# Optimization experiments

Measured on AMD Instinct MI355X. Metric: run time of the kernel, lower is better.

## Reference

```python
import jax, jax.numpy as jnp
import numpy as np
import math

B, S, D, H, NB = 32, 512, 512, 8, 2
DK = D // H
DF = 4 * D
EPS = 1e-8


def layer_norm(x, gamma, beta):
    # Matches torch: unbiased std (ddof=1), divide by (std + eps)
    mean = jnp.mean(x, axis=-1, keepdims=True)
    std = jnp.sqrt(jnp.var(x, axis=-1, keepdims=True, ddof=1))
    return gamma * (x - mean) / (std + EPS) + beta


def block(x, wq, bq, wk, bk, wv, bv, wr, br, ga, ba, wc1, bc1, wc2, bc2, gf, bf):
    # --- attention with ReLU-gated Q/K/V ---
    Q = jax.nn.relu(x @ wq.T + bq)  # [B,S,D]
    K = jax.nn.relu(x @ wk.T + bk)
    V = jax.nn.relu(x @ wv.T + bv)
    # chunk along last dim -> heads; head-major stacking is equivalent to this reshape
    Qh = Q.reshape(B, S, H, DK)
    Kh = K.reshape(B, S, H, DK)
    Vh = V.reshape(B, S, H, DK)
    scores = jnp.einsum('bqhd,bkhd->bhqk', Qh, Kh) / math.sqrt(DK)
    w = jax.nn.softmax(scores, axis=-1)
    out = jnp.einsum('bhqk,bkhd->bqhd', w, Vh).reshape(B, S, D)
    out = out + jax.nn.relu(x @ wr.T + br)
    out = layer_norm(out, ga, ba)
    # --- conv1d (kernel=1) feed-forward ---
    h = jax.nn.relu(out @ wc1.T + bc1)  # [B,S,4D]
    y = h @ wc2.T + bc2                 # [B,S,D]
    y = layer_norm(y + out, gf, bf)
    return y


def setup_inputs() -> dict:
    key = jax.random.key(0)
    ks = jax.random.split(key, 8)
    std = 0.01
    inp = {
        'x': jax.random.normal(ks[0], (B, S, D), jnp.float32),
        'wq': jax.random.normal(ks[1], (NB, D, D), jnp.float32) * std,
        'bq': jnp.zeros((NB, D), jnp.float32),
        'wk': jax.random.normal(ks[2], (NB, D, D), jnp.float32) * std,
        'bk': jnp.zeros((NB, D), jnp.float32),
        'wv': jax.random.normal(ks[3], (NB, D, D), jnp.float32) * std,
        'bv': jnp.zeros((NB, D), jnp.float32),
        'wr': jax.random.normal(ks[4], (NB, D, D), jnp.float32) * std,
        'br': jnp.zeros((NB, D), jnp.float32),
        'g_attn': jnp.ones((NB, D), jnp.float32),
        'b_attn': jnp.zeros((NB, D), jnp.float32),
        'wc1': jax.random.normal(ks[5], (NB, DF, D), jnp.float32) * (1.0 / math.sqrt(D)),
        'bc1': jnp.zeros((NB, DF), jnp.float32),
        'wc2': jax.random.normal(ks[6], (NB, D, DF), jnp.float32) * (1.0 / math.sqrt(DF)),
        'bc2': jnp.zeros((NB, D), jnp.float32),
        'g_ffn': jnp.ones((NB, D), jnp.float32),
        'b_ffn': jnp.zeros((NB, D), jnp.float32),
    }
    return inp


def reference(x, wq, bq, wk, bk, wv, bv, wr, br, g_attn, b_attn,
              wc1, bc1, wc2, bc2, g_ffn, b_ffn):
    enc = x
    for i in range(NB):
        enc = block(enc, wq[i], bq[i], wk[i], bk[i], wv[i], bv[i], wr[i], br[i],
                    g_attn[i], b_attn[i], wc1[i], bc1[i], wc2[i], bc2[i],
                    g_ffn[i], b_ffn[i])
    return enc
```

## Files before the change

kernel.cpp:

```cpp
#include <hip/hip_runtime.h>

typedef unsigned short u16;
typedef __bf16 bf16x8 __attribute__((ext_vector_type(8)));
typedef float f32x4 __attribute__((ext_vector_type(4)));
typedef unsigned short ushort8 __attribute__((ext_vector_type(8)));

__device__ __forceinline__ void gload_lds16(const void* g, void* l) {
  __builtin_amdgcn_global_load_lds(
      (const __attribute__((address_space(1))) void*)g,
      (__attribute__((address_space(3))) void*)l, 16, 0, 0);
}

__device__ __forceinline__ u16 f2bf(float f) {
  unsigned int u = __builtin_bit_cast(unsigned int, f);
  u = (u + 0x7fffu + ((u >> 16) & 1u)) >> 16;
  return (u16)u;
}
__device__ __forceinline__ u16 f2bf_trunc(float f) {
  return (u16)(__builtin_bit_cast(unsigned int, f) >> 16);
}
__device__ __forceinline__ float bf2f(u16 u) {
  unsigned int v = (unsigned int)u << 16;
  return __builtin_bit_cast(float, v);
}

__global__ void castk(const float* __restrict__ in, u16* __restrict__ out, int n,
                      float scale) {
  size_t i = ((size_t)blockIdx.x * 256 + threadIdx.x) * 8;
  if (i >= (size_t)n) return;
  const float4* p = (const float4*)(in + i);
  float4 a = p[0], b = p[1];
  ushort8 o;
  o[0] = f2bf(a.x * scale); o[1] = f2bf(a.y * scale);
  o[2] = f2bf(a.z * scale); o[3] = f2bf(a.w * scale);
  o[4] = f2bf(b.x * scale); o[5] = f2bf(b.y * scale);
  o[6] = f2bf(b.z * scale); o[7] = f2bf(b.w * scale);
  *(ushort8*)(out + i) = o;
}

__global__ void castw4(const float* __restrict__ w0, const float* __restrict__ w1,
                       const float* __restrict__ w2, const float* __restrict__ w3,
                       u16* __restrict__ out) {
  size_t idx = ((size_t)blockIdx.x * 256 + threadIdx.x) * 8;
  int i = (int)(idx >> 20);
  int j = (int)((idx >> 18) & 3);
  int e = (int)(idx & 262143);
  const float* src = (j == 0) ? w0 : (j == 1) ? w1 : (j == 2) ? w2 : w3;
  float scale = (j == 0) ? 0.125f : 1.0f;
  const float4* p = (const float4*)(src + (size_t)i * 262144 + e);
  float4 a = p[0], b = p[1];
  ushort8 o;
  o[0] = f2bf(a.x * scale); o[1] = f2bf(a.y * scale);
  o[2] = f2bf(a.z * scale); o[3] = f2bf(a.w * scale);
  o[4] = f2bf(b.x * scale); o[5] = f2bf(b.y * scale);
  o[6] = f2bf(b.z * scale); o[7] = f2bf(b.w * scale);
  *(ushort8*)(out + idx) = o;
}

__global__ void biasg(const float* __restrict__ b0, const float* __restrict__ b1,
                      const float* __restrict__ b2, const float* __restrict__ b3,
                      float* __restrict__ out) {
  int idx = blockIdx.x * 256 + threadIdx.x;
  int i = idx >> 11, j = (idx >> 9) & 3, c = idx & 511;
  const float* src = (j == 0) ? b0 : (j == 1) ? b1 : (j == 2) ? b2 : b3;
  float v = src[i * 512 + c];
  out[idx] = (j == 0) ? v * 0.125f : v;
}

template<int RELU, int WVT>
__global__ __launch_bounds__(256, 4)
void gemm97(const u16* __restrict__ A, const u16* __restrict__ W,
            const float* __restrict__ bias, u16* __restrict__ C,
            u16* __restrict__ VT, int M, int N, int K)
{
  __shared__ char lds[32768];
  char* ABase = lds;
  char* BBase = lds + 16384;

  const int tid = threadIdx.x, w = tid >> 6, l = tid & 63;
  const int l15 = l & 15, lh = l >> 4;
  const int nbn = N >> 7;
  const int p = blockIdx.x;
  const int bm = (p & 7) * 16 + (p >> 3) / nbn;
  const int bn = (p >> 3) % nbn;
  const int wm = w >> 1, wn = w & 1;
  const int NT = K >> 6;

  const int srow = l >> 3;
  const int scol = ((l & 7) ^ srow) << 3;
  const u16* aG = A + (size_t)(bm * 128 + srow) * K + scol;
  const u16* bG = W + (size_t)(bn * 128 + srow) * K + scol;

  auto stage = [&](int t) {
#pragma unroll
    for (int i = 0; i < 4; ++i) {
      int c = w * 4 + i;
      gload_lds16(aG + (size_t)(c * 8) * K + t * 64, ABase + c * 1024);
      gload_lds16(bG + (size_t)(c * 8) * K + t * 64, BBase + c * 1024);
    }
  };

  f32x4 acc[4][4] = {};

  for (int t = 0; t < NT; ++t) {
    __syncthreads();
    stage(t);
    __syncthreads();
    bf16x8 a[4], b[4];
#pragma unroll
    for (int kk = 0; kk < 2; ++kk) {
#pragma unroll
      for (int mf = 0; mf < 4; ++mf) {
        int row = wm * 64 + mf * 16 + l15;
        a[mf] = *(const bf16x8*)(ABase + row * 128 +
                 ((kk * 64 + lh * 16) ^ ((row & 7) << 4)));
      }
#pragma unroll
      for (int nf = 0; nf < 4; ++nf) {
        int row = wn * 64 + nf * 16 + l15;
        b[nf] = *(const bf16x8*)(BBase + row * 128 +
                 ((kk * 64 + lh * 16) ^ ((row & 7) << 4)));
      }
      __builtin_amdgcn_s_setprio(1);
#pragma unroll
      for (int mf = 0; mf < 4; ++mf)
#pragma unroll
        for (int nf = 0; nf < 4; ++nf)
          acc[mf][nf] = __builtin_amdgcn_mfma_f32_16x16x32_bf16(a[mf], b[nf], acc[mf][nf], 0, 0, 0);
      __builtin_amdgcn_s_setprio(0);
    }
  }

  __syncthreads();
  char* Ct = (char*)lds;
  const int rowL = wm * 64 + (lh << 2);
  const int colL = wn * 64 + l15;
  const bool dovt = WVT && (bn >= 8) && (bn < 12);
  float bv[4];
#pragma unroll
  for (int nf = 0; nf < 4; ++nf) bv[nf] = bias[bn * 128 + colL + nf * 16];

  if (!dovt) {
#pragma unroll
    for (int mf = 0; mf < 4; ++mf)
#pragma unroll
      for (int nf = 0; nf < 4; ++nf)
#pragma unroll
        for (int r = 0; r < 4; ++r) {
          float v = acc[mf][nf][r] + bv[nf];
          if (RELU) v = fmaxf(v, 0.f);
          int m = rowL + mf * 16 + r, n = colL + nf * 16;
          *(u16*)(Ct + m * 256 + ((n * 2) ^ ((m & 7) << 4))) = f2bf(v);
        }
    __syncthreads();
#pragma unroll
    for (int pass = 0; pass < 8; ++pass) {
      int row = pass * 16 + (tid >> 4);
      int c16 = tid & 15;
      bf16x8 vv = *(const bf16x8*)(Ct + row * 256 + ((c16 * 16) ^ ((row & 7) << 4)));
      *(bf16x8*)(&C[(size_t)(bm * 128 + row) * N + bn * 128 + c16 * 8]) = vv;
    }
  } else {
#pragma unroll
    for (int mf = 0; mf < 4; ++mf)
#pragma unroll
      for (int nf = 0; nf < 4; ++nf)
#pragma unroll
        for (int r = 0; r < 4; ++r) {
          float v = acc[mf][nf][r] + bv[nf];
          if (RELU) v = fmaxf(v, 0.f);
          int m = rowL + mf * 16 + r, d = colL + nf * 16;
          *(u16*)(Ct + d * 256 + ((m * 2) ^ ((d & 7) << 4))) = f2bf(v);
        }
    __syncthreads();
    const int batch = bm >> 2;
#pragma unroll
    for (int pass = 0; pass < 8; ++pass) {
      int dL = pass * 16 + (tid >> 4);
      int m16 = tid & 15;
      bf16x8 vv = *(const bf16x8*)(Ct + dL * 256 + ((m16 * 16) ^ ((dL & 7) << 4)));
      int head = (bn - 8) * 2 + (dL >> 6);
      int vtr = (batch * 8 + head) * 64 + (dL & 63);
      *(bf16x8*)(&VT[(size_t)vtr * 512 + (bm & 3) * 128 + m16 * 8]) = vv;
    }
  }
}

__global__ __launch_bounds__(256, 3)
void attn_kernel(const u16* __restrict__ qkvr, const u16* __restrict__ VT,
                 u16* __restrict__ F)
{
  const int D4 = 2048;
  __shared__ u16 QPs[128 * 64];
  __shared__ u16 Ks[2][64 * 64];
  __shared__ u16 Vs[2][64 * 64];

  const int tid = threadIdx.x, w = tid >> 6, l = tid & 63;
  const int bh = blockIdx.x & 255, qt = blockIdx.x >> 8;
  const int b = bh >> 3, h = bh & 7;
  const int lr = l >> 3, lc = ((l & 7) ^ lr) << 3;
  const int l15 = l & 15, lh = l >> 4;

  const u16* qG = qkvr + (size_t)(b * 512 + qt * 128) * D4 + h * 64 + lc;
#pragma unroll
  for (int i = 0; i < 4; ++i) {
    int c = w * 4 + i;
    gload_lds16(qG + (size_t)(c * 8 + lr) * D4, &QPs[c * 512]);
  }

  const u16* kG = qkvr + (size_t)(b * 512) * D4 + 512 + h * 64 + lc;
  const u16* vG = VT + (size_t)(bh * 64) * 512 + lc;

  auto stageKV = [&](int kt) {
    const int bsel = kt & 1;
#pragma unroll
    for (int i = 0; i < 2; ++i) {
      int c = w * 2 + i;
      gload_lds16(kG + (size_t)(kt * 64 + c * 8 + lr) * D4, &Ks[bsel][c * 512]);
      gload_lds16(vG + (size_t)(c * 8 + lr) * 512 + kt * 64, &Vs[bsel][c * 512]);
    }
  };
  stageKV(0);
  __syncthreads();

  bf16x8 qa[2][2];
#pragma unroll
  for (int kk = 0; kk < 2; ++kk)
#pragma unroll
    for (int qq = 0; qq < 2; ++qq) {
      int qrow = w * 32 + qq * 16 + l15;
      qa[kk][qq] = *(const bf16x8*)((const char*)QPs + qrow * 128 +
                    ((kk * 64 + (lh << 4)) ^ ((qrow & 7) << 4)));
    }

  f32x4 o_acc[2][4] = {};
  float psum[2][4] = {};

  for (int kt = 0; kt < 8; ++kt) {
    if (kt) __syncthreads();
    if (kt < 7) stageKV(kt + 1);
    const char* Kb = (const char*)Ks[kt & 1];
    const char* Vb = (const char*)Vs[kt & 1];

    f32x4 sacc[2][4] = {};
#pragma unroll
    for (int kk = 0; kk < 2; ++kk) {
#pragma unroll
      for (int ni = 0; ni < 4; ++ni) {
        int krow = ni * 16 + l15;
        bf16x8 kb = *(const bf16x8*)(Kb + krow * 128 +
                    ((kk * 64 + (lh << 4)) ^ ((krow & 7) << 4)));
#pragma unroll
        for (int qq = 0; qq < 2; ++qq)
          sacc[qq][ni] = __builtin_amdgcn_mfma_f32_16x16x32_bf16(qa[kk][qq], kb, sacc[qq][ni], 0, 0, 0);
      }
    }

#pragma unroll
    for (int qq = 0; qq < 2; ++qq)
#pragma unroll
      for (int r = 0; r < 4; ++r) {
        float p0 = __expf(sacc[qq][0][r]);
        float p1 = __expf(sacc[qq][1][r]);
        float p2 = __expf(sacc[qq][2][r]);
        float p3 = __expf(sacc[qq][3][r]);
        psum[qq][r] += (p0 + p1) + (p2 + p3);
        int q = w * 32 + qq * 16 + (lh << 2) + r;
        int sw = (q & 7) << 4;
        int col = l15 * 2;
        char* pb = (char*)QPs + q * 128;
        *(u16*)(pb + ((0  + col) ^ sw)) = f2bf_trunc(p0);
        *(u16*)(pb + ((32 + col) ^ sw)) = f2bf_trunc(p1);
        *(u16*)(pb + ((64 + col) ^ sw)) = f2bf_trunc(p2);
        *(u16*)(pb + ((96 + col) ^ sw)) = f2bf_trunc(p3);
      }

#pragma unroll
    for (int kk = 0; kk < 2; ++kk) {
      bf16x8 pa[2];
#pragma unroll
      for (int qq = 0; qq < 2; ++qq) {
        int qrow = w * 32 + qq * 16 + l15;
        pa[qq] = *(const bf16x8*)((const char*)QPs + qrow * 128 +
                  ((kk * 64 + (lh << 4)) ^ ((qrow & 7) << 4)));
      }
#pragma unroll
      for (int ni = 0; ni < 4; ++ni) {
        int d = ni * 16 + l15;
        bf16x8 vb = *(const bf16x8*)(Vb + d * 128 +
                    ((kk * 64 + (lh << 4)) ^ ((d & 7) << 4)));
#pragma unroll
        for (int qq = 0; qq < 2; ++qq)
          o_acc[qq][ni] = __builtin_amdgcn_mfma_f32_16x16x32_bf16(pa[qq], vb, o_acc[qq][ni], 0, 0, 0);
      }
    }
  }

  float lsum[2][4];
#pragma unroll
  for (int qq = 0; qq < 2; ++qq)
#pragma unroll
    for (int r = 0; r < 4; ++r) {
      float t = psum[qq][r];
#pragma unroll
      for (int m = 1; m < 16; m <<= 1) t += __shfl_xor(t, m);
      lsum[qq][r] = 1.f / t;
    }

#pragma unroll
  for (int qq = 0; qq < 2; ++qq)
#pragma unroll
    for (int ni = 0; ni < 4; ++ni) {
      int d = ni * 16 + l15;
#pragma unroll
      for (int r = 0; r < 4; ++r) {
        float v = o_acc[qq][ni][r] * lsum[qq][r];
        int q = w * 32 + qq * 16 + (lh << 2) + r;
        *(u16*)((char*)QPs + q * 128 + ((d * 2) ^ ((q & 7) << 4))) = f2bf(v);
      }
    }
  __syncthreads();
  const u16* Rbase = qkvr + (size_t)(b * 512 + qt * 128) * D4 + 1536 + h * 64;
  u16* Fbase = F + (size_t)(b * 512 + qt * 128) * 512 + h * 64;
#pragma unroll
  for (int pass = 0; pass < 4; ++pass) {
    int row = pass * 32 + (tid >> 3), c8 = tid & 7;
    ushort8 lv = *(const ushort8*)((char*)QPs + row * 128 + ((c8 * 16) ^ ((row & 7) << 4)));
    ushort8 rv = *(const ushort8*)(Rbase + (size_t)row * D4 + c8 * 8);
    ushort8 o;
#pragma unroll
    for (int j = 0; j < 8; ++j) o[j] = f2bf(bf2f(lv[j]) + bf2f(rv[j]));
    *(ushort8*)(Fbase + (size_t)row * 512 + c8 * 8) = o;
  }
}

template<int HAS_RES, int OUT_F32>
__global__ __launch_bounds__(256)
void ln_bf(const u16* __restrict__ in, const u16* __restrict__ res,
           const float* __restrict__ gamma, const float* __restrict__ beta,
           u16* __restrict__ outb, float* __restrict__ outf)
{
  const int l = threadIdx.x & 63;
  const size_t row = (size_t)blockIdx.x * 4 + (threadIdx.x >> 6);
  ushort8 iv = *(const ushort8*)(in + row * 512 + l * 8);
  float x[8];
#pragma unroll
  for (int j = 0; j < 8; ++j) x[j] = bf2f(iv[j]);
  if (HAS_RES) {
    ushort8 rv = *(const ushort8*)(res + row * 512 + l * 8);
#pragma unroll
    for (int j = 0; j < 8; ++j) x[j] += bf2f(rv[j]);
  }
  float s = 0.f, ss = 0.f;
#pragma unroll
  for (int j = 0; j < 8; ++j) { s += x[j]; ss += x[j] * x[j]; }
#pragma unroll
  for (int m = 1; m < 64; m <<= 1) { s += __shfl_xor(s, m); ss += __shfl_xor(ss, m); }
  float mean = s * (1.f / 512.f);
  float var = fmaxf((ss - 512.f * mean * mean) * (1.f / 511.f), 0.f);
  float inv = 1.f / (sqrtf(var) + 1e-8f);
  const float4* g4 = (const float4*)gamma;
  const float4* b4 = (const float4*)beta;
  float4 g0 = g4[l * 2], g1 = g4[l * 2 + 1];
  float4 b0 = b4[l * 2], b1 = b4[l * 2 + 1];
  float gg[8] = {g0.x, g0.y, g0.z, g0.w, g1.x, g1.y, g1.z, g1.w};
  float bb[8] = {b0.x, b0.y, b0.z, b0.w, b1.x, b1.y, b1.z, b1.w};
  float y[8];
#pragma unroll
  for (int j = 0; j < 8; ++j) y[j] = gg[j] * (x[j] - mean) * inv + bb[j];
  if (outb) {
    ushort8 o;
#pragma unroll
    for (int j = 0; j < 8; ++j) o[j] = f2bf(y[j]);
    *(ushort8*)(outb + row * 512 + l * 8) = o;
  }
  if (OUT_F32) {
    float4* o4 = (float4*)(outf + row * 512);
    o4[l * 2]     = make_float4(y[0], y[1], y[2], y[3]);
    o4[l * 2 + 1] = make_float4(y[4], y[5], y[6], y[7]);
  }
}

extern "C" void kernel_launch(void* const* d_in, const int* in_sizes, int n_in,
                              void* d_out, int out_size, void* d_ws, size_t ws_size,
                              hipStream_t stream)
{
  const int B = 32, S = 512, D = 512, NB = 2, DF = 2048;
  const int M = B * S;

  const float* x   = (const float*)d_in[0];
  const float* ga  = (const float*)d_in[9];
  const float* ba  = (const float*)d_in[10];
  const float* wc1 = (const float*)d_in[11];
  const float* bc1 = (const float*)d_in[12];
  const float* wc2 = (const float*)d_in[13];
  const float* bc2 = (const float*)d_in[14];
  const float* gf  = (const float*)d_in[15];
  const float* bfp = (const float*)d_in[16];

  char* ws = (char*)d_ws;
  u16*   curb = (u16*)(ws + 0);
  u16*   qkvr = (u16*)(ws + 16777216);
  u16*   F    = (u16*)(ws + 83886080);
  u16*   Hg   = (u16*)(ws + 100663296);
  u16*   VT   = (u16*)(ws + 117440512);
  u16*   w4b  = (u16*)(ws + 134217728);
  u16*   wc1b = (u16*)(ws + 138412032);
  u16*   wc2b = (u16*)(ws + 142606336);
  float* b4   = (float*)(ws + 146800640);
  u16*   Ih   = qkvr;
  u16*   Y    = F;

  castk<<<M * D / 2048, 256, 0, stream>>>(x, curb, M * D, 1.0f);
  castw4<<<1024, 256, 0, stream>>>((const float*)d_in[1], (const float*)d_in[3],
                                   (const float*)d_in[5], (const float*)d_in[7], w4b);
  biasg<<<16, 256, 0, stream>>>((const float*)d_in[2], (const float*)d_in[4],
                                (const float*)d_in[6], (const float*)d_in[8], b4);
  castk<<<NB * DF * D / 2048, 256, 0, stream>>>(wc1, wc1b, NB * DF * D, 1.0f);
  castk<<<NB * DF * D / 2048, 256, 0, stream>>>(wc2, wc2b, NB * DF * D, 1.0f);

  for (int i = 0; i < NB; ++i) {
    const size_t wfo = (size_t)i * DF * D;
    gemm97<1, 1><<<128 * 16, 256, 0, stream>>>(curb, w4b + (size_t)i * 1048576,
                                               b4 + i * 2048, qkvr, VT, M, 2048, 512);
    attn_kernel<<<4 * 256, 256, 0, stream>>>(qkvr, VT, F);
    ln_bf<0, 0><<<M / 4, 256, 0, stream>>>(F, nullptr, ga + i * D, ba + i * D, Hg, nullptr);
    gemm97<1, 0><<<128 * 16, 256, 0, stream>>>(Hg, wc1b + wfo, bc1 + i * DF,
                                               Ih, nullptr, M, 2048, 512);
    gemm97<0, 0><<<128 * 4, 256, 0, stream>>>(Ih, wc2b + wfo, bc2 + i * D,
                                              Y, nullptr, M, 512, 2048);
    if (i == NB - 1)
      ln_bf<1, 1><<<M / 4, 256, 0, stream>>>(Y, Hg, gf + i * D, bfp + i * D,
                                             nullptr, (float*)d_out);
    else
      ln_bf<1, 0><<<M / 4, 256, 0, stream>>>(Y, Hg, gf + i * D, bfp + i * D,
                                             curb, nullptr);
  }
}
```

Baseline: 358.0 us.

## Process two query tiles per attention block to reuse staged K/V

```diff
diff --git a/kernel.cpp b/kernel.cpp
--- a/kernel.cpp
+++ b/kernel.cpp
@@ -196,21 +196,22 @@
   __shared__ u16 Vs[2][64 * 64];
 
   const int tid = threadIdx.x, w = tid >> 6, l = tid & 63;
-  const int bh = blockIdx.x & 255, qt = blockIdx.x >> 8;
+  const int bh = blockIdx.x & 255, qp = blockIdx.x >> 8;
   const int b = bh >> 3, h = bh & 7;
   const int lr = l >> 3, lc = ((l & 7) ^ lr) << 3;
   const int l15 = l & 15, lh = l >> 4;
 
-  const u16* qG = qkvr + (size_t)(b * 512 + qt * 128) * D4 + h * 64 + lc;
-#pragma unroll
-  for (int i = 0; i < 4; ++i) {
-    int c = w * 4 + i;
-    gload_lds16(qG + (size_t)(c * 8 + lr) * D4, &QPs[c * 512]);
-  }
-
+  const u16* qG = qkvr + (size_t)(b * 512 + qp * 256) * D4 + h * 64 + lc;
   const u16* kG = qkvr + (size_t)(b * 512) * D4 + 512 + h * 64 + lc;
   const u16* vG = VT + (size_t)(bh * 64) * 512 + lc;
 
+  auto stageQ = [&](int t) {
+#pragma unroll
+    for (int i = 0; i < 4; ++i) {
+      int c = w * 4 + i;
+      gload_lds16(qG + (size_t)(t * 128 + c * 8 + lr) * D4, &QPs[c * 512]);
+    }
+  };
   auto stageKV = [&](int kt) {
     const int bsel = kt & 1;
 #pragma unroll
@@ -220,21 +221,34 @@
       gload_lds16(vG + (size_t)(c * 8 + lr) * 512 + kt * 64, &Vs[bsel][c * 512]);
     }
   };
+
+  bf16x8 qa[2][2][2];
+
+  stageQ(0);
   stageKV(0);
   __syncthreads();
-
-  bf16x8 qa[2][2];
 #pragma unroll
   for (int kk = 0; kk < 2; ++kk)
 #pragma unroll
     for (int qq = 0; qq < 2; ++qq) {
       int qrow = w * 32 + qq * 16 + l15;
-      qa[kk][qq] = *(const bf16x8*)((const char*)QPs + qrow * 128 +
-                    ((kk * 64 + (lh << 4)) ^ ((qrow & 7) << 4)));
-    }
-
-  f32x4 o_acc[2][4] = {};
-  float psum[2][4] = {};
+      qa[0][kk][qq] = *(const bf16x8*)((const char*)QPs + qrow * 128 +
+                       ((kk * 64 + (lh << 4)) ^ ((qrow & 7) << 4)));
+    }
+  __syncthreads();
+  stageQ(1);
+  __syncthreads();
+#pragma unroll
+  for (int kk = 0; kk < 2; ++kk)
+#pragma unroll
+    for (int qq = 0; qq < 2; ++qq) {
+      int qrow = w * 32 + qq * 16 + l15;
+      qa[1][kk][qq] = *(const bf16x8*)((const char*)QPs + qrow * 128 +
+                       ((kk * 64 + (lh << 4)) ^ ((qrow & 7) << 4)));
+    }
+
+  f32x4 o_acc[2][2][4] = {};
+  float psum[2][2][4] = {};
 
   for (int kt = 0; kt < 8; ++kt) {
     if (kt) __syncthreads();
@@ -242,95 +256,104 @@
     const char* Kb = (const char*)Ks[kt & 1];
     const char* Vb = (const char*)Vs[kt & 1];
 
-    f32x4 sacc[2][4] = {};
-#pragma unroll
-    for (int kk = 0; kk < 2; ++kk) {
-#pragma unroll
-      for (int ni = 0; ni < 4; ++ni) {
-        int krow = ni * 16 + l15;
-        bf16x8 kb = *(const bf16x8*)(Kb + krow * 128 +
-                    ((kk * 64 + (lh << 4)) ^ ((krow & 7) << 4)));
-#pragma unroll
-        for (int qq = 0; qq < 2; ++qq)
-          sacc[qq][ni] = __builtin_amdgcn_mfma_f32_16x16x32_bf16(qa[kk][qq], kb, sacc[qq][ni], 0, 0, 0);
-      }
-    }
-
+#pragma unroll
+    for (int qt = 0; qt < 2; ++qt) {
+      f32x4 sacc[2][4] = {};
+#pragma unroll
+      for (int kk = 0; kk < 2; ++kk) {
+#pragma unroll
+        for (int ni = 0; ni < 4; ++ni) {
+          int krow = ni * 16 + l15;
+          bf16x8 kb = *(const bf16x8*)(Kb + krow * 128 +
+                      ((kk * 64 + (lh << 4)) ^ ((krow & 7) << 4)));
+#pragma unroll
+          for (int qq = 0; qq < 2; ++qq)
+            sacc[qq][ni] = __builtin_amdgcn_mfma_f32_16x16x32_bf16(qa[qt][kk][qq], kb, sacc[qq][ni], 0, 0, 0);
+        }
+      }
+
+#pragma unroll
+      for (int qq = 0; qq < 2; ++qq)
+#pragma unroll
+        for (int r = 0; r < 4; ++r) {
+          float p0 = __expf(sacc[qq][0][r]);
+          float p1 = __expf(sacc[qq][1][r]);
+          float p2 = __expf(sacc[qq][2][r]);
+          float p3 = __expf(sacc[qq][3][r]);
+          psum[qt][qq][r] += (p0 + p1) + (p2 + p3);
+          int q = w * 32 + qq * 16 + (lh << 2) + r;
+          int sw = (q & 7) << 4;
+          int col = l15 * 2;
+          char* pb = (char*)QPs + q * 128;
+          *(u16*)(pb + ((0  + col) ^ sw)) = f2bf_trunc(p0);
+          *(u16*)(pb + ((32 + col) ^ sw)) = f2bf_trunc(p1);
+          *(u16*)(pb + ((64 + col) ^ sw)) = f2bf_trunc(p2);
+          *(u16*)(pb + ((96 + col) ^ sw)) = f2bf_trunc(p3);
+        }
+
+#pragma unroll
+      for (int kk = 0; kk < 2; ++kk) {
+        bf16x8 pa[2];
+#pragma unroll
+        for (int qq = 0; qq < 2; ++qq) {
+          int qrow = w * 32 + qq * 16 + l15;
+          pa[qq] = *(const bf16x8*)((const char*)QPs + qrow * 128 +
+                    ((kk * 64 + (lh << 4)) ^ ((qrow & 7) << 4)));
+        }
+#pragma unroll
+        for (int ni = 0; ni < 4; ++ni) {
+          int d = ni * 16 + l15;
+          bf16x8 vb = *(const bf16x8*)(Vb + d * 128 +
+                      ((kk * 64 + (lh << 4)) ^ ((d & 7) << 4)));
+#pragma unroll
+          for (int qq = 0; qq < 2; ++qq)
+            o_acc[qt][qq][ni] = __builtin_amdgcn_mfma_f32_16x16x32_bf16(pa[qq], vb, o_acc[qt][qq][ni], 0, 0, 0);
+        }
+      }
+    }
+  }
+
+  float lsum[2][2][4];
+#pragma unroll
+  for (int qt = 0; qt < 2; ++qt)
 #pragma unroll
     for (int qq = 0; qq < 2; ++qq)
 #pragma unroll
       for (int r = 0; r < 4; ++r) {
-        float p0 = __expf(sacc[qq][0][r]);
-        float p1 = __expf(sacc[qq][1][r]);
-        float p2 = __expf(sacc[qq][2][r]);
-        float p3 = __expf(sacc[qq][3][r]);
-        psum[qq][r] += (p0 + p1) + (p2 + p3);
-        int q = w * 32 + qq * 16 + (lh << 2) + r;
-        int sw = (q & 7) << 4;
-        int col = l15 * 2;
-        char* pb = (char*)QPs + q * 128;
-        *(u16*)(pb + ((0  + col) ^ sw)) = f2bf_trunc(p0);
-        *(u16*)(pb + ((32 + col) ^ sw)) = f2bf_trunc(p1);
-        *(u16*)(pb + ((64 + col) ^ sw)) = f2bf_trunc(p2);
-        *(u16*)(pb + ((96 + col) ^ sw)) = f2bf_trunc(p3);
-      }
-
-#pragma unroll
-    for (int kk = 0; kk < 2; ++kk) {
-      bf16x8 pa[2];
-#pragma unroll
-      for (int qq = 0; qq < 2; ++qq) {
-        int qrow = w * 32 + qq * 16 + l15;
-        pa[qq] = *(const bf16x8*)((const char*)QPs + qrow * 128 +
-                  ((kk * 64 + (lh << 4)) ^ ((qrow & 7) << 4)));
-      }
+        float t = psum[qt][qq][r];
+#pragma unroll
+        for (int m = 1; m < 16; m <<= 1) t += __shfl_xor(t, m);
+        lsum[qt][qq][r] = 1.f / t;
+      }
+
+#pragma unroll
+  for (int qt = 0; qt < 2; ++qt) {
+    if (qt) __syncthreads();
+#pragma unroll
+    for (int qq = 0; qq < 2; ++qq)
 #pragma unroll
       for (int ni = 0; ni < 4; ++ni) {
         int d = ni * 16 + l15;
-        bf16x8 vb = *(const bf16x8*)(Vb + d * 128 +
-                    ((kk * 64 + (lh << 4)) ^ ((d & 7) << 4)));
-#pragma unroll
-        for (int qq = 0; qq < 2; ++qq)
-          o_acc[qq][ni] = __builtin_amdgcn_mfma_f32_16x16x32_bf16(pa[qq], vb, o_acc[qq][ni], 0, 0, 0);
-      }
-    }
-  }
-
-  float lsum[2][4];
-#pragma unroll
-  for (int qq = 0; qq < 2; ++qq)
-#pragma unroll
-    for (int r = 0; r < 4; ++r) {
-      float t = psum[qq][r];
-#pragma unroll
-      for (int m = 1; m < 16; m <<= 1) t += __shfl_xor(t, m);
-      lsum[qq][r] = 1.f / t;
-    }
-
-#pragma unroll
-  for (int qq = 0; qq < 2; ++qq)
-#pragma unroll
-    for (int ni = 0; ni < 4; ++ni) {
-      int d = ni * 16 + l15;
-#pragma unroll
-      for (int r = 0; r < 4; ++r) {
-        float v = o_acc[qq][ni][r] * lsum[qq][r];
-        int q = w * 32 + qq * 16 + (lh << 2) + r;
-        *(u16*)((char*)QPs + q * 128 + ((d * 2) ^ ((q & 7) << 4))) = f2bf(v);
-      }
-    }
-  __syncthreads();
-  const u16* Rbase = qkvr + (size_t)(b * 512 + qt * 128) * D4 + 1536 + h * 64;
-  u16* Fbase = F + (size_t)(b * 512 + qt * 128) * 512 + h * 64;
-#pragma unroll
-  for (int pass = 0; pass < 4; ++pass) {
-    int row = pass * 32 + (tid >> 3), c8 = tid & 7;
-    ushort8 lv = *(const ushort8*)((char*)QPs + row * 128 + ((c8 * 16) ^ ((row & 7) << 4)));
-    ushort8 rv = *(const ushort8*)(Rbase + (size_t)row * D4 + c8 * 8);
-    ushort8 o;
-#pragma unroll
-    for (int j = 0; j < 8; ++j) o[j] = f2bf(bf2f(lv[j]) + bf2f(rv[j]));
-    *(ushort8*)(Fbase + (size_t)row * 512 + c8 * 8) = o;
+#pragma unroll
+        for (int r = 0; r < 4; ++r) {
+          float v = o_acc[qt][qq][ni][r] * lsum[qt][qq][r];
+          int q = w * 32 + qq * 16 + (lh << 2) + r;
+          *(u16*)((char*)QPs + q * 128 + ((d * 2) ^ ((q & 7) << 4))) = f2bf(v);
+        }
+      }
+    __syncthreads();
+    const u16* Rbase = qkvr + (size_t)(b * 512 + qp * 256 + qt * 128) * D4 + 1536 + h * 64;
+    u16* Fbase = F + (size_t)(b * 512 + qp * 256 + qt * 128) * 512 + h * 64;
+#pragma unroll
+    for (int pass = 0; pass < 4; ++pass) {
+      int row = pass * 32 + (tid >> 3), c8 = tid & 7;
+      ushort8 lv = *(const ushort8*)((char*)QPs + row * 128 + ((c8 * 16) ^ ((row & 7) << 4)));
+      ushort8 rv = *(const ushort8*)(Rbase + (size_t)row * D4 + c8 * 8);
+      ushort8 o;
+#pragma unroll
+      for (int j = 0; j < 8; ++j) o[j] = f2bf(bf2f(lv[j]) + bf2f(rv[j]));
+      *(ushort8*)(Fbase + (size_t)row * 512 + c8 * 8) = o;
+    }
   }
 }
 
@@ -423,7 +446,7 @@
     const size_t wfo = (size_t)i * DF * D;
     gemm97<1, 1><<<128 * 16, 256, 0, stream>>>(curb, w4b + (size_t)i * 1048576,
                                                b4 + i * 2048, qkvr, VT, M, 2048, 512);
-    attn_kernel<<<4 * 256, 256, 0, stream>>>(qkvr, VT, F);
+    attn_kernel<<<2 * 256, 256, 0, stream>>>(qkvr, VT, F);
     ln_bf<0, 0><<<M / 4, 256, 0, stream>>>(F, nullptr, ga + i * D, ba + i * D, Hg, nullptr);
     gemm97<1, 0><<<128 * 16, 256, 0, stream>>>(Hg, wc1b + wfo, bc1 + i * DF,
                                                Ih, nullptr, M, 2048, 512);
```

After: 436.6 us. 22.0% more time.
